# Performance work log

Measured on AMD Instinct MI355X. Metric: run time of the kernel, lower is better.

The kernel has to match this reference:

```python
import jax, jax.numpy as jnp
import numpy as np

C = 512          # channels
NH = 8           # num_heads
ENC = 512        # encoder_channels
SCALE_P = 1.0    # channels_scale_for_positional_embedding
CP = int(C * SCALE_P)
GROUPS = 32


def group_norm(x, g, b, eps=1e-5):
    # x: (N, C, L); GroupNorm32 computes stats in fp32
    N, Ch, L = x.shape
    xg = x.reshape(N, GROUPS, Ch // GROUPS, L).astype(jnp.float32)
    mu = xg.mean(axis=(2, 3), keepdims=True)
    var = xg.var(axis=(2, 3), keepdims=True)
    xn = ((xg - mu) * jax.lax.rsqrt(var + eps)).reshape(N, Ch, L).astype(x.dtype)
    return xn * g[None, :, None] + b[None, :, None]


def conv1(x, W, b):
    # 1x1 conv1d: x (N, Cin, L), W (Cout, Cin), b (Cout)
    return jnp.einsum('oc,ncl->nol', W, x) + b[None, :, None]


def setup_inputs() -> dict:
    key = jax.random.key(0)
    ks = iter(jax.random.split(key, 40))
    rn = lambda *s: jax.random.normal(next(ks), s, dtype=jnp.float32)
    inp = {
        'x': rn(8, C, 32, 32),
        'xf_out': rn(8, ENC, 64),
        'obj_contour_embedding': rn(8, ENC, 64),
        'obj_description_embedding': rn(8, ENC, 64),
        'image_patch_contour_embedding': rn(8, ENC, 1024),
        # norm_for_qkv
        'gn_qkv_g': jnp.ones(C), 'gn_qkv_b': jnp.zeros(C),
        # projectors (1x1 conv weights); zero_module proj_out given random weights for a meaningful baseline
        'W_self_qkv': rn(3 * C, C) * 0.02, 'b_self_qkv': jnp.zeros(3 * C),
        'W_cross_q': rn(C, C) * 0.02, 'b_cross_q': jnp.zeros(C),
        'W_content': rn(2 * C, ENC) * 0.02, 'b_content': jnp.zeros(2 * C),
        'W_pos': rn(CP, ENC) * 0.02, 'b_pos': jnp.zeros(CP),
        'gn_desc_g': jnp.ones(ENC), 'gn_desc_b': jnp.zeros(ENC),
        'gn_cpos_g': jnp.ones(CP), 'gn_cpos_b': jnp.zeros(CP),
        'gn_ipos_g': jnp.ones(CP), 'gn_ipos_b': jnp.zeros(CP),
        'W_self_out': rn(C, C) * 0.02, 'b_self_out': jnp.zeros(C),
        'W_cross_out': rn(C, C) * 0.02, 'b_cross_out': jnp.zeros(C),
    }
    return inp


def _attn(q, k, v, scale):
    # q,k: (B, Cq, T/S), v: (B, Cv, S)
    w = jnp.einsum('bct,bcs->bts', q * scale, k * scale)
    w = jax.nn.softmax(w.astype(jnp.float32), axis=-1).astype(q.dtype)
    return jnp.einsum('bts,bcs->bct', w, v)


def reference(x, xf_out, obj_contour_embedding, obj_description_embedding,
              image_patch_contour_embedding,
              gn_qkv_g, gn_qkv_b, W_self_qkv, b_self_qkv, W_cross_q, b_cross_q,
              W_content, b_content, W_pos, b_pos,
              gn_desc_g, gn_desc_b, gn_cpos_g, gn_cpos_b, gn_ipos_g, gn_ipos_b,
              W_self_out, b_self_out, W_cross_out, b_cross_out):
    b_, c_, h_, w_ = x.shape
    xf = x.reshape(b_, c_, -1)                      # (N, C, L1)
    L1 = xf.shape[-1]
    L2 = obj_contour_embedding.shape[-1]
    dc = C // NH
    dp = CP // NH
    scale = float(int((1 + SCALE_P) * C) // NH) ** -0.25

    # ---- self-attention over image patches ----
    qkv = conv1(group_norm(xf, gn_qkv_g, gn_qkv_b), W_self_qkv, b_self_qkv)
    sq, sk, sv = jnp.split(qkv, 3, axis=1)
    sq = sq.reshape(b_ * NH, dc, L1)
    sk = sk.reshape(b_ * NH, dc, L1)
    sv = sv.reshape(b_ * NH, dc, L1)

    ipos = conv1(image_patch_contour_embedding, W_pos, b_pos)
    ipos = group_norm(ipos, gn_ipos_g, gn_ipos_b)
    ipos = ipos.reshape(b_ * NH, dp, L1)

    sq = jnp.concatenate([sq, ipos], axis=1)
    sk = jnp.concatenate([sk, ipos], axis=1)
    self_out = _attn(sq, sk, sv, scale).reshape(b_, C, L1)
    self_out = conv1(self_out, W_self_out, b_self_out)
    xf = xf + self_out

    # ---- cross-attention to object tokens ----
    cq = conv1(group_norm(xf, gn_qkv_g, gn_qkv_b), W_cross_q, b_cross_q)
    cq = cq.reshape(b_ * NH, dc, L1)
    cq = jnp.concatenate([cq, ipos], axis=1)

    cpos = conv1(obj_contour_embedding, W_pos, b_pos)
    cpos = group_norm(cpos, gn_cpos_g, gn_cpos_b)
    cpos = cpos.reshape(b_ * NH, dp, L2)

    content = (xf_out + group_norm(obj_description_embedding, gn_desc_g, gn_desc_b)) / 2
    kv = conv1(content, W_content, b_content)
    ck, cv = jnp.split(kv, 2, axis=1)
    ck = ck.reshape(b_ * NH, dc, L2)
    cv = cv.reshape(b_ * NH, dc, L2)
    ck = jnp.concatenate([ck, cpos], axis=1)

    cross_out = _attn(cq, ck, cv, scale).reshape(b_, C, L1)
    cross_out = conv1(cross_out, W_cross_out, b_cross_out)

    return (xf + cross_out).reshape(b_, c_, h_, w_)
```

## Files before the change

kernel.cpp:

```cpp
#include <hip/hip_runtime.h>

typedef unsigned short u16;
typedef __attribute__((ext_vector_type(8))) short bf16x8;
typedef __attribute__((ext_vector_type(4))) float f32x4;

__device__ __forceinline__ float bf2f(u16 u) {
  union { unsigned int i; float f; } v;
  v.i = ((unsigned int)u) << 16;
  return v.f;
}
__device__ __forceinline__ u16 f2bf(float f) {
  union { float f; unsigned int i; } v;
  v.f = f;
  unsigned int r = v.i + 0x7FFFu + ((v.i >> 16) & 1u);
  return (u16)(r >> 16);
}
__device__ __forceinline__ unsigned int cvtpk(float lo, float hi) {
  unsigned int r;
  asm("v_cvt_pk_bf16_f32 %0, %1, %2" : "=v"(r) : "v"(lo), "v"(hi));
  return r;
}

__device__ __forceinline__ float4 ld4f(const float* p) {
  return *reinterpret_cast<const float4*>(p);
}
__device__ __forceinline__ float4 ld4f(const u16* p) {
  uint2 v = *reinterpret_cast<const uint2*>(p);
  float4 r;
  r.x = bf2f((u16)(v.x & 0xffff)); r.y = bf2f((u16)(v.x >> 16));
  r.z = bf2f((u16)(v.y & 0xffff)); r.w = bf2f((u16)(v.y >> 16));
  return r;
}

template <typename TIN>
__global__ __launch_bounds__(1024) void gn_kernel(
    const TIN* __restrict__ In, u16* __restrict__ OutBuf,
    const float* __restrict__ G, const float* __restrict__ Bt,
    const float* __restrict__ Add, float post_scale,
    int C, int L, int cpg)
{
  const int blk = blockIdx.x;
  const int n = blk >> 5, grp = blk & 31;
  const size_t base = ((size_t)n * C + (size_t)grp * cpg) * L;
  const int cnt = cpg * L;
  const int cnt4 = cnt >> 2;
  const int tid = threadIdx.x;

  float s = 0.f, s2 = 0.f;
  for (int i = tid; i < cnt4; i += 1024) {
    float4 v = ld4f(In + base + (size_t)i * 4);
    s += v.x + v.y + v.z + v.w;
    s2 += v.x * v.x + v.y * v.y + v.z * v.z + v.w * v.w;
  }
#pragma unroll
  for (int d = 1; d < 64; d <<= 1) {
    s += __shfl_xor(s, d);
    s2 += __shfl_xor(s2, d);
  }
  __shared__ float ps[16], ps2[16], stat[2];
  const int wid = tid >> 6;
  if ((tid & 63) == 0) { ps[wid] = s; ps2[wid] = s2; }
  __syncthreads();
  if (tid == 0) {
    float a = 0.f, b2 = 0.f;
#pragma unroll
    for (int w = 0; w < 16; ++w) { a += ps[w]; b2 += ps2[w]; }
    const float mean = a / cnt;
    const float var = b2 / cnt - mean * mean;
    stat[0] = mean;
    stat[1] = rsqrtf(var + 1e-5f);
  }
  __syncthreads();
  const float mean = stat[0], rstd = stat[1];

  for (int i = tid; i < cnt4; i += 1024) {
    const int i4 = i * 4;
    const int ch = grp * cpg + i4 / L;
    float4 v = ld4f(In + base + i4);
    const float g = G[ch] * rstd, bt = Bt[ch] - mean * rstd * G[ch];
    float4 r;
    r.x = v.x * g + bt; r.y = v.y * g + bt;
    r.z = v.z * g + bt; r.w = v.w * g + bt;
    if (Add) {
      float4 a = *reinterpret_cast<const float4*>(Add + base + i4);
      r.x = (r.x + a.x) * post_scale; r.y = (r.y + a.y) * post_scale;
      r.z = (r.z + a.z) * post_scale; r.w = (r.w + a.w) * post_scale;
    }
    uint2 o;
    o.x = (unsigned int)f2bf(r.x) | ((unsigned int)f2bf(r.y) << 16);
    o.y = (unsigned int)f2bf(r.z) | ((unsigned int)f2bf(r.w) << 16);
    *reinterpret_cast<uint2*>(OutBuf + base + i4) = o;
  }
}

__device__ __forceinline__ void loadpair4(const u16* p0, const u16* p1,
                                          unsigned int* bw) {
  uint2 a = *reinterpret_cast<const uint2*>(p0);
  uint2 c = *reinterpret_cast<const uint2*>(p1);
  bw[0] = (a.x & 0xffffu) | (c.x << 16);
  bw[1] = (a.x >> 16) | (c.x & 0xffff0000u);
  bw[2] = (a.y & 0xffffu) | (c.y << 16);
  bw[3] = (a.y >> 16) | (c.y & 0xffff0000u);
}
__device__ __forceinline__ void loadpair4(const float* p0, const float* p1,
                                          unsigned int* bw) {
  float4 a = *reinterpret_cast<const float4*>(p0);
  float4 c = *reinterpret_cast<const float4*>(p1);
  bw[0] = cvtpk(a.x, c.x); bw[1] = cvtpk(a.y, c.y);
  bw[2] = cvtpk(a.z, c.z); bw[3] = cvtpk(a.w, c.w);
}

template <typename TX>
__global__ __launch_bounds__(256) void gemm_small(
    const TX* __restrict__ X, const float* __restrict__ W,
    const float* __restrict__ Bias,
    u16* __restrict__ OutBf,
    int Cin, int L, int O)
{
  __shared__ __align__(16) u16 As[64][40];
  __shared__ __align__(16) u16 Bs[64][40];
  const int tid = threadIdx.x;
  const int wave = tid >> 6;
  const int lane = tid & 63;
  const int n = blockIdx.z;
  const int o0 = blockIdx.x * 64;
  const int l0 = blockIdx.y * 64;
  const TX* Xn = X + (size_t)n * Cin * L;

  const int ao = tid >> 2, akc = (tid & 3) * 8;
  const int c2 = (tid & 15) * 2, lt0 = (tid >> 4) * 4;
  const float* wp = W + (size_t)(o0 + ao) * Cin + akc;
  const TX* xp0 = Xn + (size_t)c2 * L + l0 + lt0;
  const TX* xp1 = xp0 + L;

  f32x4 acc[4];
#pragma unroll
  for (int i = 0; i < 4; ++i) acc[i] = (f32x4){0.f, 0.f, 0.f, 0.f};

  const int row = lane & 15;
  const int kh = (lane >> 4) * 8;

  float4 wa = *reinterpret_cast<const float4*>(wp);
  float4 wb = *reinterpret_cast<const float4*>(wp + 4);
  unsigned int bw[4];
  loadpair4(xp0, xp1, bw);

  const int nK = Cin >> 5;
  for (int kt = 0; kt < nK; ++kt) {
    {
      uint4 ap;
      ap.x = cvtpk(wa.x, wa.y); ap.y = cvtpk(wa.z, wa.w);
      ap.z = cvtpk(wb.x, wb.y); ap.w = cvtpk(wb.z, wb.w);
      *reinterpret_cast<uint4*>(&As[ao][akc]) = ap;
    }
#pragma unroll
    for (int j = 0; j < 4; ++j)
      *reinterpret_cast<unsigned int*>(&Bs[lt0 + j][c2]) = bw[j];
    __syncthreads();

    if (kt + 1 < nK) {
      const int k0 = (kt + 1) * 32;
      wa = *reinterpret_cast<const float4*>(wp + k0);
      wb = *reinterpret_cast<const float4*>(wp + k0 + 4);
      loadpair4(xp0 + (size_t)k0 * L, xp1 + (size_t)k0 * L, bw);
    }

    bf16x8 a = *reinterpret_cast<const bf16x8*>(&As[wave * 16 + row][kh]);
#pragma unroll
    for (int lt = 0; lt < 4; ++lt) {
      bf16x8 b = *reinterpret_cast<const bf16x8*>(&Bs[lt * 16 + row][kh]);
      acc[lt] = __builtin_amdgcn_mfma_f32_16x16x32_bf16(a, b, acc[lt], 0, 0, 0);
    }
    __syncthreads();
  }

  const int col = lane & 15;
  const int r0 = (lane >> 4) * 4;
#pragma unroll
  for (int lt = 0; lt < 4; ++lt) {
    const int ll = l0 + lt * 16 + col;
#pragma unroll
    for (int j = 0; j < 4; ++j) {
      const int oo = o0 + wave * 16 + r0 + j;
      float v = acc[lt][j] + Bias[oo];
      OutBf[((size_t)n * O + oo) * L + ll] = f2bf(v);
    }
  }
}

template <typename TX>
__global__ __launch_bounds__(512) void gemm_big(
    const TX* __restrict__ X, const float* __restrict__ W,
    const float* __restrict__ Bias,
    u16* __restrict__ OutBf, float* __restrict__ Out32,
    const float* __restrict__ Res,
    int Cin, int L, int O, int mode)
{
  __shared__ __align__(16) u16 As[128][40];
  __shared__ __align__(16) u16 Bs[128][40];
  const int tid = threadIdx.x;
  const int wave = tid >> 6;
  const int lane = tid & 63;
  const int n = blockIdx.z;
  const int o0 = blockIdx.x * 128;
  const int l0 = blockIdx.y * 128;
  const TX* Xn = X + (size_t)n * Cin * L;

  const int ao = tid >> 2, akc = (tid & 3) * 8;
  const int c2 = (tid & 15) * 2, lt0 = (tid >> 4) * 4;
  const float* wp = W + (size_t)(o0 + ao) * Cin + akc;
  const TX* xp0 = Xn + (size_t)c2 * L + l0 + lt0;
  const TX* xp1 = xp0 + L;

  f32x4 acc[8];
#pragma unroll
  for (int i = 0; i < 8; ++i) acc[i] = (f32x4){0.f, 0.f, 0.f, 0.f};

  const int row = lane & 15;
  const int kh = (lane >> 4) * 8;

  float4 wa = *reinterpret_cast<const float4*>(wp);
  float4 wb = *reinterpret_cast<const float4*>(wp + 4);
  unsigned int bw[4];
  loadpair4(xp0, xp1, bw);

  const int nK = Cin >> 5;
  for (int kt = 0; kt < nK; ++kt) {
    {
      uint4 ap;
      ap.x = cvtpk(wa.x, wa.y); ap.y = cvtpk(wa.z, wa.w);
      ap.z = cvtpk(wb.x, wb.y); ap.w = cvtpk(wb.z, wb.w);
      *reinterpret_cast<uint4*>(&As[ao][akc]) = ap;
    }
#pragma unroll
    for (int j = 0; j < 4; ++j)
      *reinterpret_cast<unsigned int*>(&Bs[lt0 + j][c2]) = bw[j];
    __syncthreads();

    if (kt + 1 < nK) {
      const int k0 = (kt + 1) * 32;
      wa = *reinterpret_cast<const float4*>(wp + k0);
      wb = *reinterpret_cast<const float4*>(wp + k0 + 4);
      loadpair4(xp0 + (size_t)k0 * L, xp1 + (size_t)k0 * L, bw);
    }

    bf16x8 a = *reinterpret_cast<const bf16x8*>(&As[wave * 16 + row][kh]);
#pragma unroll
    for (int lt = 0; lt < 8; ++lt) {
      bf16x8 b = *reinterpret_cast<const bf16x8*>(&Bs[lt * 16 + row][kh]);
      acc[lt] = __builtin_amdgcn_mfma_f32_16x16x32_bf16(a, b, acc[lt], 0, 0, 0);
    }
    __syncthreads();
  }

  const int col = lane & 15;
  const int r0 = (lane >> 4) * 4;
#pragma unroll
  for (int lt = 0; lt < 8; ++lt) {
    const int ll = l0 + lt * 16 + col;
#pragma unroll
    for (int j = 0; j < 4; ++j) {
      const int oo = o0 + wave * 16 + r0 + j;
      float v = acc[lt][j] + Bias[oo];
      const size_t idx = ((size_t)n * O + oo) * L + ll;
      if (mode == 1) {
        Out32[idx] = v + Res[idx];
      } else {
        OutBf[idx] = f2bf(v);
      }
    }
  }
}

__global__ __launch_bounds__(256, 2) void flash_attn(
    const u16* __restrict__ qA, int qA_C, int qA_off,
    const u16* __restrict__ qB,
    const u16* __restrict__ kA, int kA_C, int kA_off,
    const u16* __restrict__ kB,
    const u16* __restrict__ V, int v_C, int v_off,
    u16* __restrict__ Out, int S_len, float qscale)
{
  __shared__ __align__(16) u16 smem[20480];
  u16* const Qs = smem;
  u16* const Ks = smem;
  u16* const Ps = smem + 8192;
  u16* const Vt = smem + 16384;

  const int tid = threadIdx.x;
  const int wave = tid >> 6, lane = tid & 63;
  const int b = blockIdx.y >> 3, h = blockIdx.y & 7;
  const int t0 = blockIdx.x * 128;
  const int l16 = lane & 15, q4 = lane >> 4;
  const int swz = (l16 & 7) << 3;

  const int c2 = (tid & 63) * 2;
  const u16* q0 = (c2 < 64)
      ? qA + ((size_t)b * qA_C + qA_off + h * 64 + c2) * 1024 + t0
      : qB + ((size_t)b * 512 + h * 64 + (c2 - 64)) * 1024 + t0;
  const u16* q1 = q0 + 1024;
  const u16* k0 = (c2 < 64)
      ? kA + ((size_t)b * kA_C + kA_off + h * 64 + c2) * (size_t)S_len
      : kB + ((size_t)b * 512 + h * 64 + (c2 - 64)) * (size_t)S_len;
  const u16* k1 = k0 + S_len;
  const u16* vb = V + ((size_t)b * v_C + v_off + h * 64) * (size_t)S_len;

  const int s8 = (tid >> 6) * 8;
  const int cv0 = tid >> 3, sb0 = (tid & 7) * 8;
  const int cv1 = (tid + 256) >> 3, sb1 = sb0;

  uint4 kr0a = *reinterpret_cast<const uint4*>(k0 + s8);
  uint4 kr0c = *reinterpret_cast<const uint4*>(k1 + s8);
  uint4 kr1a = *reinterpret_cast<const uint4*>(k0 + s8 + 32);
  uint4 kr1c = *reinterpret_cast<const uint4*>(k1 + s8 + 32);
  uint4 vr0 = *reinterpret_cast<const uint4*>(vb + (size_t)cv0 * S_len + sb0);
  uint4 vr1 = *reinterpret_cast<const uint4*>(vb + (size_t)cv1 * S_len + sb1);

#pragma unroll
  for (int it = 0; it < 4; ++it) {
    const int t8 = (tid >> 6) * 8 + it * 32;
    union { uint4 q; u16 u[8]; } a, c;
    a.q = *reinterpret_cast<const uint4*>(q0 + t8);
    c.q = *reinterpret_cast<const uint4*>(q1 + t8);
#pragma unroll
    for (int j = 0; j < 8; ++j) {
      const unsigned int w =
          cvtpk(bf2f(a.u[j]) * qscale, bf2f(c.u[j]) * qscale);
      *reinterpret_cast<unsigned int*>(&Qs[(t8 + j) * 128 + (c2 ^ (j << 3))]) = w;
    }
  }
  __syncthreads();

  bf16x8 qf[2][4];
#pragma unroll
  for (int g = 0; g < 2; ++g)
#pragma unroll
    for (int kk = 0; kk < 4; ++kk)
      qf[g][kk] = *reinterpret_cast<const bf16x8*>(
          &Qs[(wave * 32 + g * 16 + l16) * 128 + ((kk * 32 + q4 * 8) ^ swz)]);
  __syncthreads();

  float m_run[2][4], l_run[2][4];
  f32x4 o_acc[2][4];
#pragma unroll
  for (int g = 0; g < 2; ++g)
#pragma unroll
    for (int j = 0; j < 4; ++j) {
      m_run[g][j] = -1e30f; l_run[g][j] = 0.f;
      o_acc[g][j] = (f32x4){0.f, 0.f, 0.f, 0.f};
    }

  const int NT = S_len >> 6;
  for (int t = 0; t < NT; ++t) {
    {
      union { uint4 q; u16 u[8]; } a, c;
      a.q = kr0a; c.q = kr0c;
#pragma unroll
      for (int j = 0; j < 8; ++j)
        *reinterpret_cast<unsigned int*>(&Ks[(s8 + j) * 128 + (c2 ^ (j << 3))]) =
            (unsigned int)a.u[j] | ((unsigned int)c.u[j] << 16);
      a.q = kr1a; c.q = kr1c;
#pragma unroll
      for (int j = 0; j < 8; ++j)
        *reinterpret_cast<unsigned int*>(&Ks[(s8 + 32 + j) * 128 + (c2 ^ (j << 3))]) =
            (unsigned int)a.u[j] | ((unsigned int)c.u[j] << 16);
    }
    *reinterpret_cast<uint4*>(&Vt[cv0 * 64 + (sb0 ^ ((cv0 & 7) << 3))]) = vr0;
    *reinterpret_cast<uint4*>(&Vt[cv1 * 64 + (sb1 ^ ((cv1 & 7) << 3))]) = vr1;
    __syncthreads();

    if (t + 1 < NT) {
      const int sc = (t + 1) * 64;
      kr0a = *reinterpret_cast<const uint4*>(k0 + sc + s8);
      kr0c = *reinterpret_cast<const uint4*>(k1 + sc + s8);
      kr1a = *reinterpret_cast<const uint4*>(k0 + sc + s8 + 32);
      kr1c = *reinterpret_cast<const uint4*>(k1 + sc + s8 + 32);
      vr0 = *reinterpret_cast<const uint4*>(vb + (size_t)cv0 * S_len + sc + sb0);
      vr1 = *reinterpret_cast<const uint4*>(vb + (size_t)cv1 * S_len + sc + sb1);
    }

    f32x4 sacc[2][4];
#pragma unroll
    for (int g = 0; g < 2; ++g)
#pragma unroll
      for (int st = 0; st < 4; ++st) sacc[g][st] = (f32x4){0.f, 0.f, 0.f, 0.f};
    __builtin_amdgcn_s_setprio(1);
#pragma unroll
    for (int st = 0; st < 4; ++st) {
#pragma unroll
      for (int kk = 0; kk < 4; ++kk) {
        bf16x8 kf = *reinterpret_cast<const bf16x8*>(
            &Ks[(st * 16 + l16) * 128 + ((kk * 32 + q4 * 8) ^ swz)]);
        sacc[0][st] = __builtin_amdgcn_mfma_f32_16x16x32_bf16(qf[0][kk], kf, sacc[0][st], 0, 0, 0);
        sacc[1][st] = __builtin_amdgcn_mfma_f32_16x16x32_bf16(qf[1][kk], kf, sacc[1][st], 0, 0, 0);
      }
    }
    __builtin_amdgcn_s_setprio(0);

#pragma unroll
    for (int g = 0; g < 2; ++g) {
      float mt[4];
#pragma unroll
      for (int j = 0; j < 4; ++j)
        mt[j] = fmaxf(fmaxf(sacc[g][0][j], sacc[g][1][j]),
                      fmaxf(sacc[g][2][j], sacc[g][3][j]));
#pragma unroll
      for (int d = 1; d < 16; d <<= 1)
#pragma unroll
        for (int j = 0; j < 4; ++j) mt[j] = fmaxf(mt[j], __shfl_xor(mt[j], d));

      float corr[4], ls[4];
#pragma unroll
      for (int j = 0; j < 4; ++j) {
        const float mn = fmaxf(m_run[g][j], mt[j]);
        corr[j] = exp2f(m_run[g][j] - mn);
        m_run[g][j] = mn;
        ls[j] = 0.f;
      }
      float pv[4][4];
#pragma unroll
      for (int st = 0; st < 4; ++st)
#pragma unroll
        for (int j = 0; j < 4; ++j) {
          pv[st][j] = exp2f(sacc[g][st][j] - m_run[g][j]);
          ls[j] += pv[st][j];
        }
#pragma unroll
      for (int d = 1; d < 16; d <<= 1)
#pragma unroll
        for (int j = 0; j < 4; ++j) ls[j] += __shfl_xor(ls[j], d);
#pragma unroll
      for (int j = 0; j < 4; ++j) l_run[g][j] = l_run[g][j] * corr[j] + ls[j];

#pragma unroll
      for (int st = 0; st < 4; ++st)
#pragma unroll
        for (int j = 0; j < 4; ++j)
          Ps[(wave * 32 + g * 16 + q4 * 4 + j) * 64 +
             ((st * 16 + l16) ^ (((q4 * 4 + j) & 7) << 3))] = f2bf(pv[st][j]);

#pragma unroll
      for (int ct = 0; ct < 4; ++ct)
#pragma unroll
        for (int j = 0; j < 4; ++j) o_acc[g][ct][j] *= corr[j];
    }

    bf16x8 pa[2][2];
#pragma unroll
    for (int g = 0; g < 2; ++g)
#pragma unroll
      for (int ks = 0; ks < 2; ++ks)
        pa[g][ks] = *reinterpret_cast<const bf16x8*>(
            &Ps[(wave * 32 + g * 16 + l16) * 64 + ((ks * 32 + q4 * 8) ^ swz)]);
    __builtin_amdgcn_s_setprio(1);
#pragma unroll
    for (int ct = 0; ct < 4; ++ct) {
#pragma unroll
      for (int ks = 0; ks < 2; ++ks) {
        bf16x8 vf = *reinterpret_cast<const bf16x8*>(
            &Vt[(ct * 16 + l16) * 64 + ((ks * 32 + q4 * 8) ^ swz)]);
        o_acc[0][ct] = __builtin_amdgcn_mfma_f32_16x16x32_bf16(pa[0][ks], vf, o_acc[0][ct], 0, 0, 0);
        o_acc[1][ct] = __builtin_amdgcn_mfma_f32_16x16x32_bf16(pa[1][ks], vf, o_acc[1][ct], 0, 0, 0);
      }
    }
    __builtin_amdgcn_s_setprio(0);
    __syncthreads();
  }

#pragma unroll
  for (int g = 0; g < 2; ++g) {
    float inv[4];
#pragma unroll
    for (int j = 0; j < 4; ++j) inv[j] = 1.f / l_run[g][j];
    const size_t obase =
        ((size_t)b * 512 + h * 64) * 1024 + t0 + wave * 32 + g * 16 + q4 * 4;
#pragma unroll
    for (int ct = 0; ct < 4; ++ct) {
      union { unsigned long long d; u16 u[4]; } pk;
#pragma unroll
      for (int j = 0; j < 4; ++j) pk.u[j] = f2bf(o_acc[g][ct][j] * inv[j]);
      *reinterpret_cast<unsigned long long*>(
          Out + obase + (size_t)(ct * 16 + l16) * 1024) = pk.d;
    }
  }
}

extern "C" void kernel_launch(void* const* d_in, const int* in_sizes, int n_in,
                              void* d_out, int out_size, void* d_ws, size_t ws_size,
                              hipStream_t stream) {
  const float* X_in        = (const float*)d_in[0];
  const float* xf_out      = (const float*)d_in[1];
  const float* obj_cont    = (const float*)d_in[2];
  const float* obj_desc    = (const float*)d_in[3];
  const float* ipce        = (const float*)d_in[4];
  const float* gn_qkv_g    = (const float*)d_in[5];
  const float* gn_qkv_b    = (const float*)d_in[6];
  const float* W_self_qkv  = (const float*)d_in[7];
  const float* b_self_qkv  = (const float*)d_in[8];
  const float* W_cross_q   = (const float*)d_in[9];
  const float* b_cross_q   = (const float*)d_in[10];
  const float* W_content   = (const float*)d_in[11];
  const float* b_content   = (const float*)d_in[12];
  const float* W_pos       = (const float*)d_in[13];
  const float* b_pos       = (const float*)d_in[14];
  const float* gn_desc_g   = (const float*)d_in[15];
  const float* gn_desc_b   = (const float*)d_in[16];
  const float* gn_cpos_g   = (const float*)d_in[17];
  const float* gn_cpos_b   = (const float*)d_in[18];
  const float* gn_ipos_g   = (const float*)d_in[19];
  const float* gn_ipos_b   = (const float*)d_in[20];
  const float* W_self_out  = (const float*)d_in[21];
  const float* b_self_out  = (const float*)d_in[22];
  const float* W_cross_out = (const float*)d_in[23];
  const float* b_cross_out = (const float*)d_in[24];

  char* base = (char*)d_ws;
  u16* A = (u16*)base;
  u16* B = (u16*)(base + 8 * 1024 * 1024);
  u16* C = (u16*)(base + 32 * 1024 * 1024);
  u16* D = (u16*)(base + 40 * 1024 * 1024);

  u16* norm1 = A;
  u16* norm2 = A;
  u16* cposr   = A;
  u16* cpos    = A + 262144;
  u16* content = A + 2 * 262144;
  u16* kvbuf   = A + 3 * 262144;
  u16* qkv  = B;
  u16* cq   = B;
  u16* ipos = C;
  u16* iposr = D;
  u16* attn1 = D;
  u16* cattn = D;
  float* xf32 = (float*)d_out;
  float* outp = (float*)d_out;

  const float qscale = 0.08838834764831845f * 1.4426950408889634f;
  dim3 blk(256);
  dim3 blkg(512);
  dim3 blkgn(1024);

  gn_kernel<float><<<dim3(256), blkgn, 0, stream>>>(X_in, norm1, gn_qkv_g, gn_qkv_b,
                                                    nullptr, 1.f, 512, 1024, 16);
  gemm_big<u16><<<dim3(12, 8, 8), blkg, 0, stream>>>(norm1, W_self_qkv, b_self_qkv,
                                                     qkv, nullptr, nullptr,
                                                     512, 1024, 1536, 0);
  gemm_big<float><<<dim3(4, 8, 8), blkg, 0, stream>>>(ipce, W_pos, b_pos, iposr,
                                                      nullptr, nullptr,
                                                      512, 1024, 512, 0);
  gn_kernel<u16><<<dim3(256), blkgn, 0, stream>>>(iposr, ipos, gn_ipos_g, gn_ipos_b,
                                                  nullptr, 1.f, 512, 1024, 16);
  flash_attn<<<dim3(8, 64), blk, 0, stream>>>(qkv, 1536, 0, ipos,
                                              qkv, 1536, 512, ipos,
                                              qkv, 1536, 1024,
                                              attn1, 1024, qscale);
  gemm_big<u16><<<dim3(4, 8, 8), blkg, 0, stream>>>(attn1, W_self_out, b_self_out,
                                                    nullptr, xf32, X_in,
                                                    512, 1024, 512, 1);
  gn_kernel<float><<<dim3(256), blkgn, 0, stream>>>(xf32, norm2, gn_qkv_g, gn_qkv_b,
                                                    nullptr, 1.f, 512, 1024, 16);
  gemm_big<u16><<<dim3(4, 8, 8), blkg, 0, stream>>>(norm2, W_cross_q, b_cross_q, cq,
                                                    nullptr, nullptr,
                                                    512, 1024, 512, 0);
  gemm_small<float><<<dim3(8, 1, 8), blk, 0, stream>>>(obj_cont, W_pos, b_pos, cposr,
                                                       512, 64, 512);
  gn_kernel<u16><<<dim3(256), blkgn, 0, stream>>>(cposr, cpos, gn_cpos_g, gn_cpos_b,
                                                  nullptr, 1.f, 512, 64, 16);
  gn_kernel<float><<<dim3(256), blkgn, 0, stream>>>(obj_desc, content, gn_desc_g,
                                                    gn_desc_b, xf_out, 0.5f, 512, 64, 16);
  gemm_small<u16><<<dim3(16, 1, 8), blk, 0, stream>>>(content, W_content, b_content,
                                                      kvbuf, 512, 64, 1024);
  flash_attn<<<dim3(8, 64), blk, 0, stream>>>(cq, 512, 0, ipos,
                                              kvbuf, 1024, 0, cpos,
                                              kvbuf, 1024, 512,
                                              cattn, 64, qscale);
  gemm_big<u16><<<dim3(4, 8, 8), blkg, 0, stream>>>(cattn, W_cross_out, b_cross_out,
                                                    nullptr, outp, xf32,
                                                    512, 1024, 512, 1);
}
```

Before: 288.8 us.

## Retile big GEMM to 64x128 tiles with K=64 per stage and 256 threads

Changes gemm_big from 512-thread 128x128 tiles with K=32 steps to 256-thread 64x128 tiles with K=64 steps, padded LDS rows and two MFMAs per B fragment per iteration. This halves the number of barrier-separated K iterations and doubles the grid size for better CU coverage. It also replaces the packed cvt_pk_bf16 instruction with scalar software f2bf rounding in both GEMMs. That adds ALU work and register pressure from the 16-element staging arrays.

```diff
diff --git a/kernel.cpp b/kernel.cpp
--- a/kernel.cpp
+++ b/kernel.cpp
@@ -93,21 +93,27 @@
   }
 }
 
-__device__ __forceinline__ void loadpair4(const u16* p0, const u16* p1,
-                                          unsigned int* bw) {
-  uint2 a = *reinterpret_cast<const uint2*>(p0);
-  uint2 c = *reinterpret_cast<const uint2*>(p1);
-  bw[0] = (a.x & 0xffffu) | (c.x << 16);
-  bw[1] = (a.x >> 16) | (c.x & 0xffff0000u);
-  bw[2] = (a.y & 0xffffu) | (c.y << 16);
-  bw[3] = (a.y >> 16) | (c.y & 0xffff0000u);
-}
-__device__ __forceinline__ void loadpair4(const float* p0, const float* p1,
-                                          unsigned int* bw) {
-  float4 a = *reinterpret_cast<const float4*>(p0);
-  float4 c = *reinterpret_cast<const float4*>(p1);
-  bw[0] = cvtpk(a.x, c.x); bw[1] = cvtpk(a.y, c.y);
-  bw[2] = cvtpk(a.z, c.z); bw[3] = cvtpk(a.w, c.w);
+__device__ __forceinline__ void load4(const u16* p, u16* d) {
+  uint2 v = *reinterpret_cast<const uint2*>(p);
+  d[0] = (u16)(v.x & 0xffff); d[1] = (u16)(v.x >> 16);
+  d[2] = (u16)(v.y & 0xffff); d[3] = (u16)(v.y >> 16);
+}
+__device__ __forceinline__ void load4(const float* p, u16* d) {
+  float4 v = *reinterpret_cast<const float4*>(p);
+  d[0] = f2bf(v.x); d[1] = f2bf(v.y); d[2] = f2bf(v.z); d[3] = f2bf(v.w);
+}
+__device__ __forceinline__ void load16(const u16* p, u16* d) {
+  union { uint4 q; u16 u[8]; } t;
+  t.q = *reinterpret_cast<const uint4*>(p);
+#pragma unroll
+  for (int i = 0; i < 8; ++i) d[i] = t.u[i];
+  t.q = *reinterpret_cast<const uint4*>(p + 8);
+#pragma unroll
+  for (int i = 0; i < 8; ++i) d[8 + i] = t.u[i];
+}
+__device__ __forceinline__ void load16(const float* p, u16* d) {
+#pragma unroll
+  for (int i = 0; i < 16; i += 4) load4(p + i, d + i);
 }
 
 template <typename TX>
@@ -142,27 +148,32 @@
 
   float4 wa = *reinterpret_cast<const float4*>(wp);
   float4 wb = *reinterpret_cast<const float4*>(wp + 4);
-  unsigned int bw[4];
-  loadpair4(xp0, xp1, bw);
+  u16 blo[4], bhi[4];
+  load4(xp0, blo);
+  load4(xp1, bhi);
 
   const int nK = Cin >> 5;
   for (int kt = 0; kt < nK; ++kt) {
     {
-      uint4 ap;
-      ap.x = cvtpk(wa.x, wa.y); ap.y = cvtpk(wa.z, wa.w);
-      ap.z = cvtpk(wb.x, wb.y); ap.w = cvtpk(wb.z, wb.w);
-      *reinterpret_cast<uint4*>(&As[ao][akc]) = ap;
+      union { uint4 q; u16 u[8]; } ap;
+      ap.u[0] = f2bf(wa.x); ap.u[1] = f2bf(wa.y);
+      ap.u[2] = f2bf(wa.z); ap.u[3] = f2bf(wa.w);
+      ap.u[4] = f2bf(wb.x); ap.u[5] = f2bf(wb.y);
+      ap.u[6] = f2bf(wb.z); ap.u[7] = f2bf(wb.w);
+      *reinterpret_cast<uint4*>(&As[ao][akc]) = ap.q;
     }
 #pragma unroll
     for (int j = 0; j < 4; ++j)
-      *reinterpret_cast<unsigned int*>(&Bs[lt0 + j][c2]) = bw[j];
+      *reinterpret_cast<unsigned int*>(&Bs[lt0 + j][c2]) =
+          (unsigned int)blo[j] | ((unsigned int)bhi[j] << 16);
     __syncthreads();
 
     if (kt + 1 < nK) {
       const int k0 = (kt + 1) * 32;
       wa = *reinterpret_cast<const float4*>(wp + k0);
       wb = *reinterpret_cast<const float4*>(wp + k0 + 4);
-      loadpair4(xp0 + (size_t)k0 * L, xp1 + (size_t)k0 * L, bw);
+      load4(xp0 + (size_t)k0 * L, blo);
+      load4(xp1 + (size_t)k0 * L, bhi);
     }
 
     bf16x8 a = *reinterpret_cast<const bf16x8*>(&As[wave * 16 + row][kh]);
@@ -189,26 +200,26 @@
 }
 
 template <typename TX>
-__global__ __launch_bounds__(512) void gemm_big(
+__global__ __launch_bounds__(256) void gemm_big(
     const TX* __restrict__ X, const float* __restrict__ W,
     const float* __restrict__ Bias,
     u16* __restrict__ OutBf, float* __restrict__ Out32,
     const float* __restrict__ Res,
     int Cin, int L, int O, int mode)
 {
-  __shared__ __align__(16) u16 As[128][40];
-  __shared__ __align__(16) u16 Bs[128][40];
+  __shared__ __align__(16) u16 As[64][72];
+  __shared__ __align__(16) u16 Bs[128][72];
   const int tid = threadIdx.x;
   const int wave = tid >> 6;
   const int lane = tid & 63;
   const int n = blockIdx.z;
-  const int o0 = blockIdx.x * 128;
+  const int o0 = blockIdx.x * 64;
   const int l0 = blockIdx.y * 128;
   const TX* Xn = X + (size_t)n * Cin * L;
 
-  const int ao = tid >> 2, akc = (tid & 3) * 8;
-  const int c2 = (tid & 15) * 2, lt0 = (tid >> 4) * 4;
-  const float* wp = W + (size_t)(o0 + ao) * Cin + akc;
+  const int ao = tid >> 2, ak = (tid & 3) * 16;
+  const int c2 = (tid & 31) * 2, lt0 = (tid >> 5) * 16;
+  const float* wp = W + (size_t)(o0 + ao) * Cin + ak;
   const TX* xp0 = Xn + (size_t)c2 * L + l0 + lt0;
   const TX* xp1 = xp0 + L;
 
@@ -219,36 +230,50 @@
   const int row = lane & 15;
   const int kh = (lane >> 4) * 8;
 
-  float4 wa = *reinterpret_cast<const float4*>(wp);
-  float4 wb = *reinterpret_cast<const float4*>(wp + 4);
-  unsigned int bw[4];
-  loadpair4(xp0, xp1, bw);
-
-  const int nK = Cin >> 5;
+  float wv[16];
+#pragma unroll
+  for (int i = 0; i < 16; i += 4) {
+    float4 v = *reinterpret_cast<const float4*>(wp + i);
+    wv[i] = v.x; wv[i + 1] = v.y; wv[i + 2] = v.z; wv[i + 3] = v.w;
+  }
+  u16 b0[16], b1[16];
+  load16(xp0, b0);
+  load16(xp1, b1);
+
+  const int nK = Cin >> 6;
   for (int kt = 0; kt < nK; ++kt) {
-    {
-      uint4 ap;
-      ap.x = cvtpk(wa.x, wa.y); ap.y = cvtpk(wa.z, wa.w);
-      ap.z = cvtpk(wb.x, wb.y); ap.w = cvtpk(wb.z, wb.w);
-      *reinterpret_cast<uint4*>(&As[ao][akc]) = ap;
-    }
-#pragma unroll
-    for (int j = 0; j < 4; ++j)
-      *reinterpret_cast<unsigned int*>(&Bs[lt0 + j][c2]) = bw[j];
+#pragma unroll
+    for (int h = 0; h < 2; ++h) {
+      union { uint4 q; u16 u[8]; } ap;
+#pragma unroll
+      for (int j = 0; j < 8; ++j) ap.u[j] = f2bf(wv[h * 8 + j]);
+      *reinterpret_cast<uint4*>(&As[ao][ak + h * 8]) = ap.q;
+    }
+#pragma unroll
+    for (int j = 0; j < 16; ++j)
+      *reinterpret_cast<unsigned int*>(&Bs[lt0 + j][c2]) =
+          (unsigned int)b0[j] | ((unsigned int)b1[j] << 16);
     __syncthreads();
 
     if (kt + 1 < nK) {
-      const int k0 = (kt + 1) * 32;
-      wa = *reinterpret_cast<const float4*>(wp + k0);
-      wb = *reinterpret_cast<const float4*>(wp + k0 + 4);
-      loadpair4(xp0 + (size_t)k0 * L, xp1 + (size_t)k0 * L, bw);
-    }
-
-    bf16x8 a = *reinterpret_cast<const bf16x8*>(&As[wave * 16 + row][kh]);
+      const int k0 = (kt + 1) * 64;
+#pragma unroll
+      for (int i = 0; i < 16; i += 4) {
+        float4 v = *reinterpret_cast<const float4*>(wp + k0 + i);
+        wv[i] = v.x; wv[i + 1] = v.y; wv[i + 2] = v.z; wv[i + 3] = v.w;
+      }
+      load16(xp0 + (size_t)k0 * L, b0);
+      load16(xp1 + (size_t)k0 * L, b1);
+    }
+
+    bf16x8 a0 = *reinterpret_cast<const bf16x8*>(&As[wave * 16 + row][kh]);
+    bf16x8 a1 = *reinterpret_cast<const bf16x8*>(&As[wave * 16 + row][kh + 32]);
 #pragma unroll
     for (int lt = 0; lt < 8; ++lt) {
-      bf16x8 b = *reinterpret_cast<const bf16x8*>(&Bs[lt * 16 + row][kh]);
-      acc[lt] = __builtin_amdgcn_mfma_f32_16x16x32_bf16(a, b, acc[lt], 0, 0, 0);
+      bf16x8 bb0 = *reinterpret_cast<const bf16x8*>(&Bs[lt * 16 + row][kh]);
+      acc[lt] = __builtin_amdgcn_mfma_f32_16x16x32_bf16(a0, bb0, acc[lt], 0, 0, 0);
+      bf16x8 bb1 = *reinterpret_cast<const bf16x8*>(&Bs[lt * 16 + row][kh + 32]);
+      acc[lt] = __builtin_amdgcn_mfma_f32_16x16x32_bf16(a1, bb1, acc[lt], 0, 0, 0);
     }
     __syncthreads();
   }
@@ -536,31 +561,30 @@
 
   const float qscale = 0.08838834764831845f * 1.4426950408889634f;
   dim3 blk(256);
-  dim3 blkg(512);
   dim3 blkgn(1024);
 
   gn_kernel<float><<<dim3(256), blkgn, 0, stream>>>(X_in, norm1, gn_qkv_g, gn_qkv_b,
                                                     nullptr, 1.f, 512, 1024, 16);
-  gemm_big<u16><<<dim3(12, 8, 8), blkg, 0, stream>>>(norm1, W_self_qkv, b_self_qkv,
-                                                     qkv, nullptr, nullptr,
-                                                     512, 1024, 1536, 0);
-  gemm_big<float><<<dim3(4, 8, 8), blkg, 0, stream>>>(ipce, W_pos, b_pos, iposr,
-                                                      nullptr, nullptr,
-                                                      512, 1024, 512, 0);
+  gemm_big<u16><<<dim3(24, 8, 8), blk, 0, stream>>>(norm1, W_self_qkv, b_self_qkv,
+                                                    qkv, nullptr, nullptr,
+                                                    512, 1024, 1536, 0);
+  gemm_big<float><<<dim3(8, 8, 8), blk, 0, stream>>>(ipce, W_pos, b_pos, iposr,
+                                                     nullptr, nullptr,
+                                                     512, 1024, 512, 0);
   gn_kernel<u16><<<dim3(256), blkgn, 0, stream>>>(iposr, ipos, gn_ipos_g, gn_ipos_b,
                                                   nullptr, 1.f, 512, 1024, 16);
   flash_attn<<<dim3(8, 64), blk, 0, stream>>>(qkv, 1536, 0, ipos,
                                               qkv, 1536, 512, ipos,
                                               qkv, 1536, 1024,
                                               attn1, 1024, qscale);
-  gemm_big<u16><<<dim3(4, 8, 8), blkg, 0, stream>>>(attn1, W_self_out, b_self_out,
-                                                    nullptr, xf32, X_in,
-                                                    512, 1024, 512, 1);
+  gemm_big<u16><<<dim3(8, 8, 8), blk, 0, stream>>>(attn1, W_self_out, b_self_out,
+                                                   nullptr, xf32, X_in,
+                                                   512, 1024, 512, 1);
   gn_kernel<float><<<dim3(256), blkgn, 0, stream>>>(xf32, norm2, gn_qkv_g, gn_qkv_b,
                                                     nullptr, 1.f, 512, 1024, 16);
-  gemm_big<u16><<<dim3(4, 8, 8), blkg, 0, stream>>>(norm2, W_cross_q, b_cross_q, cq,
-                                                    nullptr, nullptr,
-                                                    512, 1024, 512, 0);
+  gemm_big<u16><<<dim3(8, 8, 8), blk, 0, stream>>>(norm2, W_cross_q, b_cross_q, cq,
+                                                   nullptr, nullptr,
+                                                   512, 1024, 512, 0);
   gemm_small<float><<<dim3(8, 1, 8), blk, 0, stream>>>(obj_cont, W_pos, b_pos, cposr,
                                                        512, 64, 512);
   gn_kernel<u16><<<dim3(256), blkgn, 0, stream>>>(cposr, cpos, gn_cpos_g, gn_cpos_b,
@@ -573,7 +597,7 @@
                                               kvbuf, 1024, 0, cpos,
                                               kvbuf, 1024, 512,
                                               cattn, 64, qscale);
-  gemm_big<u16><<<dim3(4, 8, 8), blkg, 0, stream>>>(cattn, W_cross_out, b_cross_out,
-                                                    nullptr, outp, xf32,
-                                                    512, 1024, 512, 1);
-}
+  gemm_big<u16><<<dim3(8, 8, 8), blk, 0, stream>>>(cattn, W_cross_out, b_cross_out,
+                                                   nullptr, outp, xf32,
+                                                   512, 1024, 512, 1);
+}
```

Result: faster. 282.8 us (-2.1%).
